# Kernel optimization log

Hardware: AMD Instinct MI355X
Metric: run time of the kernel (lower is better)

## Reference

```python
import jax, jax.numpy as jnp
import numpy as np

IN_FEATURES = 2048
N_CONCEPTS = 64
EMB_SIZE = 128
BATCH = 8192
NEG_SLOPE = 0.01  # torch LeakyReLU default


def _leaky_relu(x):
    return jnp.where(x >= 0, x, NEG_SLOPE * x)


def setup_inputs() -> dict:
    key = jax.random.key(0)
    ks = jax.random.split(key, 7)
    s_e = 1.0 / np.sqrt(IN_FEATURES)
    s_c = 1.0 / np.sqrt(EMB_SIZE)
    s_p = 1.0 / np.sqrt(2 * EMB_SIZE)
    return {
        "x": jax.random.normal(ks[0], (BATCH, IN_FEATURES), jnp.float32),
        # embedder: Linear(in_features, emb_size)
        "We": jax.random.uniform(ks[1], (EMB_SIZE, IN_FEATURES), jnp.float32, -s_e, s_e),
        "be": jax.random.uniform(ks[2], (EMB_SIZE,), jnp.float32, -s_e, s_e),
        # per-concept generators: K x Linear(emb_size, 2*emb_size)
        "Wc": jax.random.uniform(ks[3], (N_CONCEPTS, 2 * EMB_SIZE, EMB_SIZE), jnp.float32, -s_c, s_c),
        "bc": jax.random.uniform(ks[4], (N_CONCEPTS, 2 * EMB_SIZE), jnp.float32, -s_c, s_c),
        # shared prob predictor: Linear(2*emb_size, 1)
        "wp": jax.random.uniform(ks[5], (2 * EMB_SIZE,), jnp.float32, -s_p, s_p),
        "bp": jax.random.uniform(ks[6], (1,), jnp.float32, -s_p, s_p),
    }


def reference(x, We, be, Wc, bc, wp, bp):
    # emb_pre: [B, E]
    emb = _leaky_relu(x @ We.T + be)
    # per-concept contexts, batched GEMM: [B, K, 2E]
    context = _leaky_relu(jnp.einsum("be,khe->bkh", emb, Wc) + bc)
    # concept probabilities: [B, K]
    c_pred = jax.nn.sigmoid(jnp.einsum("bkh,h->bk", context, wp) + bp[0])
    # no interventions (c=None) -> c_int == c_pred
    c_int = c_pred
    context_pos = context[:, :, :EMB_SIZE]
    context_neg = context[:, :, EMB_SIZE:]
    g = c_pred[:, :, None]
    c_emb = context_pos * g + context_neg * (1.0 - g)  # [B, K, E]
    return c_emb, c_pred, c_int, emb
```

## Files before the change

kernel.cpp:

```cpp
#include <hip/hip_runtime.h>
#include <hip/hip_bf16.h>

#define IN_F   2048
#define N_CON  64
#define EMB    128
#define BATCH  8192

#define CEMB_OFF  0
#define CPRED_OFF 67108864
#define CINT_OFF  67633152
#define EMB_OFF   68157440

typedef __attribute__((ext_vector_type(4))) float f32x4;
typedef __attribute__((ext_vector_type(8))) short short8;
typedef __attribute__((ext_vector_type(4))) short short4v;

#define MFMA16(A,B,C) __builtin_amdgcn_mfma_f32_16x16x32_bf16((A),(B),(C),0,0,0)

__device__ __forceinline__ short f2bf(float f) {
  unsigned u = __float_as_uint(f);
  u += 0x7FFFu + ((u >> 16) & 1u);
  return (short)(u >> 16);
}

__device__ __forceinline__ void gload_lds16(const void* g, void* l) {
  __builtin_amdgcn_global_load_lds(
      (const __attribute__((address_space(1))) unsigned*)g,
      (__attribute__((address_space(3))) unsigned*)l, 16, 0, 0);
}

__global__ void conv2_kernel(const float* __restrict__ a, short* __restrict__ da, int n4a,
                             const float* __restrict__ b, short* __restrict__ db, int n4b) {
  int i = blockIdx.x * blockDim.x + threadIdx.x;
  const float* s; short* d; int j;
  if (i < n4a)            { s = a; d = da; j = i; }
  else if (i < n4a + n4b) { s = b; d = db; j = i - n4a; }
  else return;
  f32x4 v = *(const f32x4*)(s + (size_t)j * 4);
  short4v o;
  o.x = f2bf(v.x); o.y = f2bf(v.y); o.z = f2bf(v.z); o.w = f2bf(v.w);
  *(short4v*)(d + (size_t)j * 4) = o;
}

__global__ __launch_bounds__(256, 4)
void gemm1_kernel(const float* __restrict__ x,
                  const short* __restrict__ we_bf,
                  const float* __restrict__ be,
                  float* __restrict__ out_emb,
                  short* __restrict__ emb_bf) {
  __shared__ short As[32 * 128];
  __shared__ short Bs[128 * 128];

  const int t = threadIdx.x;
  const int w = t >> 6, l = t & 63;
  const int row0 = blockIdx.x * 32;

  f32x4 acc[2][2];
#pragma unroll
  for (int i = 0; i < 2; ++i)
#pragma unroll
    for (int j = 0; j < 2; ++j) acc[i][j] = (f32x4){0.f, 0.f, 0.f, 0.f};

  const int ar = t >> 3;
  const int as = t & 7;
  const float* xrow = x + (size_t)(row0 + ar) * IN_F + as * 16;

  const int brl = t >> 4;
  const int bseg = l & 15;

  for (int kt = 0; kt < 16; ++kt) {
    const int k0 = kt * 128;
#pragma unroll
    for (int h = 0; h < 2; ++h) {
      f32x4 v0 = *(const f32x4*)(xrow + k0 + h * 8);
      f32x4 v1 = *(const f32x4*)(xrow + k0 + h * 8 + 4);
      short8 o;
      o[0] = f2bf(v0.x); o[1] = f2bf(v0.y); o[2] = f2bf(v0.z); o[3] = f2bf(v0.w);
      o[4] = f2bf(v1.x); o[5] = f2bf(v1.y); o[6] = f2bf(v1.z); o[7] = f2bf(v1.w);
      int col = (as * 16 + h * 8) ^ ((ar & 7) << 3);
      *(short8*)&As[ar * 128 + col] = o;
    }
#pragma unroll
    for (int i = 0; i < 8; ++i) {
      int n = i * 16 + brl;
      const short* src = we_bf + (size_t)n * IN_F + k0 + ((bseg ^ (n & 7)) * 8);
      gload_lds16(src, &Bs[i * 2048 + w * 512]);
    }
    __syncthreads();
#pragma unroll
    for (int ks = 0; ks < 4; ++ks) {
      int kcol = ks * 32 + ((l >> 4) << 3);
      int r0 = l & 15, r1 = 16 + (l & 15);
      short8 a0 = *(const short8*)&As[r0 * 128 + (kcol ^ ((r0 & 7) << 3))];
      short8 a1 = *(const short8*)&As[r1 * 128 + (kcol ^ ((r1 & 7) << 3))];
      int n0 = w * 32 + (l & 15), n1 = w * 32 + 16 + (l & 15);
      short8 b0 = *(const short8*)&Bs[n0 * 128 + (kcol ^ ((n0 & 7) << 3))];
      short8 b1 = *(const short8*)&Bs[n1 * 128 + (kcol ^ ((n1 & 7) << 3))];
      acc[0][0] = MFMA16(a0, b0, acc[0][0]);
      acc[1][0] = MFMA16(a1, b0, acc[1][0]);
      acc[0][1] = MFMA16(a0, b1, acc[0][1]);
      acc[1][1] = MFMA16(a1, b1, acc[1][1]);
    }
    __syncthreads();
  }

#pragma unroll
  for (int nf = 0; nf < 2; ++nf) {
    int e = w * 32 + nf * 16 + (l & 15);
    float bev = be[e];
#pragma unroll
    for (int mf = 0; mf < 2; ++mf) {
#pragma unroll
      for (int r = 0; r < 4; ++r) {
        int b = row0 + mf * 16 + ((l >> 4) << 2) + r;
        float v = acc[mf][nf][r] + bev;
        v = v >= 0.f ? v : 0.01f * v;
        out_emb[(size_t)b * EMB + e] = v;
        emb_bf[(size_t)b * EMB + e] = f2bf(v);
      }
    }
  }
}

__global__ __launch_bounds__(512, 2)
void gemm2_kernel(const short* __restrict__ emb_bf,
                  const short* __restrict__ wc_bf,
                  const float* __restrict__ bc,
                  const float* __restrict__ wp,
                  const float* __restrict__ bp,
                  float* __restrict__ ws_pred,
                  float* __restrict__ out) {
  __shared__ short As[256 * 128];
  __shared__ short Bs[256 * 128];

  const int t = threadIdx.x;
  const int w = t >> 6, l = t & 63;
  const int kc = blockIdx.x & 63;
  const int mbase = (blockIdx.x >> 6) * 256;

  float wph[16], bcv[16];
#pragma unroll
  for (int nf = 0; nf < 16; ++nf) {
    wph[nf] = wp[nf * 16 + (l & 15)];
    bcv[nf] = bc[kc * 256 + nf * 16 + (l & 15)];
  }
  const float bp0 = bp[0];

  const int rl = t >> 4;
  const int seg = l & 15;
#pragma unroll
  for (int i = 0; i < 8; ++i) {
    int rA = i * 32 + rl;
    gload_lds16(emb_bf + (size_t)(mbase + rA) * 128 + ((seg ^ (rA & 7)) * 8),
                &As[i * 4096 + w * 512]);
  }
#pragma unroll
  for (int i = 0; i < 8; ++i) {
    int rB = i * 32 + rl;
    gload_lds16(wc_bf + (size_t)kc * 32768 + (size_t)rB * 128 + ((seg ^ (rB & 7)) * 8),
                &Bs[i * 4096 + w * 512]);
  }
  __syncthreads();

  f32x4 acc[2][16];
#pragma unroll
  for (int i = 0; i < 2; ++i)
#pragma unroll
    for (int j = 0; j < 16; ++j) acc[i][j] = (f32x4){0.f, 0.f, 0.f, 0.f};

  const int wr = w * 32;
#pragma unroll
  for (int ks = 0; ks < 4; ++ks) {
    int kcol = ks * 32 + ((l >> 4) << 3);
    int r0 = wr + (l & 15), r1 = wr + 16 + (l & 15);
    short8 a0 = *(const short8*)&As[r0 * 128 + (kcol ^ ((r0 & 7) << 3))];
    short8 a1 = *(const short8*)&As[r1 * 128 + (kcol ^ ((r1 & 7) << 3))];
#pragma unroll
    for (int nf = 0; nf < 16; ++nf) {
      int n = nf * 16 + (l & 15);
      short8 b = *(const short8*)&Bs[n * 128 + (kcol ^ ((n & 7) << 3))];
      acc[0][nf] = MFMA16(a0, b, acc[0][nf]);
      acc[1][nf] = MFMA16(a1, b, acc[1][nf]);
    }
  }

  float g[2][4];
#pragma unroll
  for (int mf = 0; mf < 2; ++mf) {
    f32x4 p = (f32x4){0.f, 0.f, 0.f, 0.f};
#pragma unroll
    for (int nf = 0; nf < 16; ++nf) {
#pragma unroll
      for (int r = 0; r < 4; ++r) {
        float v = acc[mf][nf][r] + bcv[nf];
        v = v >= 0.f ? v : 0.01f * v;
        acc[mf][nf][r] = v;
        p[r] += v * wph[nf];
      }
    }
#pragma unroll
    for (int r = 0; r < 4; ++r) {
      float s = p[r];
      s += __shfl_xor(s, 1);
      s += __shfl_xor(s, 2);
      s += __shfl_xor(s, 4);
      s += __shfl_xor(s, 8);
      g[mf][r] = 1.f / (1.f + __expf(-(s + bp0)));
    }
  }

  if ((l & 15) == 0) {
#pragma unroll
    for (int mf = 0; mf < 2; ++mf) {
      f32x4 gv;
      gv.x = g[mf][0]; gv.y = g[mf][1]; gv.z = g[mf][2]; gv.w = g[mf][3];
      *(f32x4*)&ws_pred[(size_t)kc * 8192 + mbase + wr + mf * 16 + ((l >> 4) << 2)] = gv;
    }
  }

#pragma unroll
  for (int mf = 0; mf < 2; ++mf) {
#pragma unroll
    for (int r = 0; r < 4; ++r) {
      int brow = mbase + wr + mf * 16 + ((l >> 4) << 2) + r;
      float gg = g[mf][r];
#pragma unroll
      for (int nf = 0; nf < 8; ++nf) {
        float v = acc[mf][nf][r] * gg + acc[mf][nf + 8][r] * (1.f - gg);
        out[(size_t)brow * 8192 + kc * 128 + nf * 16 + (l & 15)] = v;
      }
    }
  }
}

__global__ __launch_bounds__(256)
void pred_tr_kernel(const float* __restrict__ ws_pred, float* __restrict__ out) {
  __shared__ float T[64][65];
  const int t = threadIdx.x;
  const int b0 = blockIdx.x * 64;

  {
    int kc = t >> 2;
    int j0 = (t & 3) * 16;
    const float* src = ws_pred + (size_t)kc * 8192 + b0 + j0;
#pragma unroll
    for (int i = 0; i < 4; ++i) {
      f32x4 v = *(const f32x4*)(src + i * 4);
      T[kc][j0 + i * 4 + 0] = v.x;
      T[kc][j0 + i * 4 + 1] = v.y;
      T[kc][j0 + i * 4 + 2] = v.z;
      T[kc][j0 + i * 4 + 3] = v.w;
    }
  }
  __syncthreads();
  {
    int bl = t & 63;
    int kq = (t >> 6) * 16;
#pragma unroll
    for (int i = 0; i < 4; ++i) {
      f32x4 v;
      v.x = T[kq + i * 4 + 0][bl];
      v.y = T[kq + i * 4 + 1][bl];
      v.z = T[kq + i * 4 + 2][bl];
      v.w = T[kq + i * 4 + 3][bl];
      *(f32x4*)&out[CPRED_OFF + (size_t)(b0 + bl) * 64 + kq + i * 4] = v;
      *(f32x4*)&out[CINT_OFF + (size_t)(b0 + bl) * 64 + kq + i * 4] = v;
    }
  }
}

extern "C" void kernel_launch(void* const* d_in, const int* in_sizes, int n_in,
                              void* d_out, int out_size, void* d_ws, size_t ws_size,
                              hipStream_t stream) {
  (void)in_sizes; (void)n_in; (void)out_size; (void)ws_size;
  const float* x  = (const float*)d_in[0];
  const float* We = (const float*)d_in[1];
  const float* be = (const float*)d_in[2];
  const float* Wc = (const float*)d_in[3];
  const float* bc = (const float*)d_in[4];
  const float* wp = (const float*)d_in[5];
  const float* bp = (const float*)d_in[6];
  float* out = (float*)d_out;

  short* we_bf  = (short*)d_ws;
  short* wc_bf  = we_bf + 262144;
  short* emb_bf = wc_bf + 2097152;
  float* ws_pred = (float*)(emb_bf + 1048576);

  conv2_kernel<<<2304, 256, 0, stream>>>(We, we_bf, 65536, Wc, wc_bf, 524288);
  gemm1_kernel<<<256, 256, 0, stream>>>(x, we_bf, be, out + EMB_OFF, emb_bf);
  gemm2_kernel<<<2048, 512, 0, stream>>>(emb_bf, wc_bf, bc, wp, bp, ws_pred, out);
  pred_tr_kernel<<<128, 256, 0, stream>>>(ws_pred, out);
}
```

Baseline: 136.5 us.

## Keep concept weight tile resident and loop over batch chunks in gemm2

gemm2 now loads each concept's 256x128 weight tile into LDS once per block and iterates over eight 64-row batch chunks, reloading only the small activation tile each iteration. Grid drops from 2048 to 1024 blocks of 256 threads with fewer accumulators per thread. gemm1 is also retiled to 16-row blocks, doubling its grid to 512 blocks for better occupancy. The point is to cut redundant weight traffic and register pressure. The cost is a serialized chunk loop with extra barriers and little overlap between the activation reload and compute.

```diff
diff --git a/kernel.cpp b/kernel.cpp
--- a/kernel.cpp
+++ b/kernel.cpp
@@ -48,58 +48,52 @@
                   const float* __restrict__ be,
                   float* __restrict__ out_emb,
                   short* __restrict__ emb_bf) {
-  __shared__ short As[32 * 128];
+  __shared__ short As[16 * 128];
   __shared__ short Bs[128 * 128];
 
   const int t = threadIdx.x;
   const int w = t >> 6, l = t & 63;
-  const int row0 = blockIdx.x * 32;
-
-  f32x4 acc[2][2];
-#pragma unroll
-  for (int i = 0; i < 2; ++i)
-#pragma unroll
-    for (int j = 0; j < 2; ++j) acc[i][j] = (f32x4){0.f, 0.f, 0.f, 0.f};
-
-  const int ar = t >> 3;
-  const int as = t & 7;
-  const float* xrow = x + (size_t)(row0 + ar) * IN_F + as * 16;
+  const int row0 = blockIdx.x * 16;
+
+  f32x4 acc[2];
+  acc[0] = (f32x4){0.f, 0.f, 0.f, 0.f};
+  acc[1] = (f32x4){0.f, 0.f, 0.f, 0.f};
+
+  const int ar = t >> 4;
+  const int aseg = t & 15;
+  const float* xrow = x + (size_t)(row0 + ar) * IN_F + aseg * 8;
+  short* adst = &As[ar * 128 + ((aseg * 8) ^ ((ar & 7) << 3))];
 
   const int brl = t >> 4;
   const int bseg = l & 15;
 
   for (int kt = 0; kt < 16; ++kt) {
     const int k0 = kt * 128;
-#pragma unroll
-    for (int h = 0; h < 2; ++h) {
-      f32x4 v0 = *(const f32x4*)(xrow + k0 + h * 8);
-      f32x4 v1 = *(const f32x4*)(xrow + k0 + h * 8 + 4);
+    {
+      f32x4 v0 = *(const f32x4*)(xrow + k0);
+      f32x4 v1 = *(const f32x4*)(xrow + k0 + 4);
       short8 o;
       o[0] = f2bf(v0.x); o[1] = f2bf(v0.y); o[2] = f2bf(v0.z); o[3] = f2bf(v0.w);
       o[4] = f2bf(v1.x); o[5] = f2bf(v1.y); o[6] = f2bf(v1.z); o[7] = f2bf(v1.w);
-      int col = (as * 16 + h * 8) ^ ((ar & 7) << 3);
-      *(short8*)&As[ar * 128 + col] = o;
+      *(short8*)adst = o;
     }
 #pragma unroll
     for (int i = 0; i < 8; ++i) {
       int n = i * 16 + brl;
-      const short* src = we_bf + (size_t)n * IN_F + k0 + ((bseg ^ (n & 7)) * 8);
-      gload_lds16(src, &Bs[i * 2048 + w * 512]);
+      gload_lds16(we_bf + (size_t)n * IN_F + k0 + ((bseg ^ (n & 7)) * 8),
+                  &Bs[i * 2048 + w * 512]);
     }
     __syncthreads();
 #pragma unroll
     for (int ks = 0; ks < 4; ++ks) {
       int kcol = ks * 32 + ((l >> 4) << 3);
-      int r0 = l & 15, r1 = 16 + (l & 15);
-      short8 a0 = *(const short8*)&As[r0 * 128 + (kcol ^ ((r0 & 7) << 3))];
-      short8 a1 = *(const short8*)&As[r1 * 128 + (kcol ^ ((r1 & 7) << 3))];
-      int n0 = w * 32 + (l & 15), n1 = w * 32 + 16 + (l & 15);
+      int r0 = l & 15;
+      short8 a = *(const short8*)&As[r0 * 128 + (kcol ^ ((r0 & 7) << 3))];
+      int n0 = w * 32 + (l & 15), n1 = n0 + 16;
       short8 b0 = *(const short8*)&Bs[n0 * 128 + (kcol ^ ((n0 & 7) << 3))];
       short8 b1 = *(const short8*)&Bs[n1 * 128 + (kcol ^ ((n1 & 7) << 3))];
-      acc[0][0] = MFMA16(a0, b0, acc[0][0]);
-      acc[1][0] = MFMA16(a1, b0, acc[1][0]);
-      acc[0][1] = MFMA16(a0, b1, acc[0][1]);
-      acc[1][1] = MFMA16(a1, b1, acc[1][1]);
+      acc[0] = MFMA16(a, b0, acc[0]);
+      acc[1] = MFMA16(a, b1, acc[1]);
     }
     __syncthreads();
   }
@@ -109,20 +103,17 @@
     int e = w * 32 + nf * 16 + (l & 15);
     float bev = be[e];
 #pragma unroll
-    for (int mf = 0; mf < 2; ++mf) {
-#pragma unroll
-      for (int r = 0; r < 4; ++r) {
-        int b = row0 + mf * 16 + ((l >> 4) << 2) + r;
-        float v = acc[mf][nf][r] + bev;
-        v = v >= 0.f ? v : 0.01f * v;
-        out_emb[(size_t)b * EMB + e] = v;
-        emb_bf[(size_t)b * EMB + e] = f2bf(v);
-      }
-    }
-  }
-}
-
-__global__ __launch_bounds__(512, 2)
+    for (int r = 0; r < 4; ++r) {
+      int b = row0 + ((l >> 4) << 2) + r;
+      float v = acc[nf][r] + bev;
+      v = v >= 0.f ? v : 0.01f * v;
+      out_emb[(size_t)b * EMB + e] = v;
+      emb_bf[(size_t)b * EMB + e] = f2bf(v);
+    }
+  }
+}
+
+__global__ __launch_bounds__(256, 2)
 void gemm2_kernel(const short* __restrict__ emb_bf,
                   const short* __restrict__ wc_bf,
                   const float* __restrict__ bc,
@@ -130,13 +121,13 @@
                   const float* __restrict__ bp,
                   float* __restrict__ ws_pred,
                   float* __restrict__ out) {
-  __shared__ short As[256 * 128];
   __shared__ short Bs[256 * 128];
+  __shared__ short As[64 * 128];
 
   const int t = threadIdx.x;
   const int w = t >> 6, l = t & 63;
   const int kc = blockIdx.x & 63;
-  const int mbase = (blockIdx.x >> 6) * 256;
+  const int mch = (blockIdx.x >> 6) * 512;
 
   float wph[16], bcv[16];
 #pragma unroll
@@ -148,56 +139,62 @@
 
   const int rl = t >> 4;
   const int seg = l & 15;
-#pragma unroll
-  for (int i = 0; i < 8; ++i) {
-    int rA = i * 32 + rl;
-    gload_lds16(emb_bf + (size_t)(mbase + rA) * 128 + ((seg ^ (rA & 7)) * 8),
-                &As[i * 4096 + w * 512]);
-  }
-#pragma unroll
-  for (int i = 0; i < 8; ++i) {
-    int rB = i * 32 + rl;
+
+#pragma unroll
+  for (int i = 0; i < 16; ++i) {
+    int rB = i * 16 + rl;
     gload_lds16(wc_bf + (size_t)kc * 32768 + (size_t)rB * 128 + ((seg ^ (rB & 7)) * 8),
-                &Bs[i * 4096 + w * 512]);
-  }
-  __syncthreads();
-
-  f32x4 acc[2][16];
-#pragma unroll
-  for (int i = 0; i < 2; ++i)
-#pragma unroll
-    for (int j = 0; j < 16; ++j) acc[i][j] = (f32x4){0.f, 0.f, 0.f, 0.f};
-
-  const int wr = w * 32;
-#pragma unroll
-  for (int ks = 0; ks < 4; ++ks) {
-    int kcol = ks * 32 + ((l >> 4) << 3);
-    int r0 = wr + (l & 15), r1 = wr + 16 + (l & 15);
-    short8 a0 = *(const short8*)&As[r0 * 128 + (kcol ^ ((r0 & 7) << 3))];
-    short8 a1 = *(const short8*)&As[r1 * 128 + (kcol ^ ((r1 & 7) << 3))];
+                &Bs[i * 2048 + w * 512]);
+  }
+#pragma unroll
+  for (int i = 0; i < 4; ++i) {
+    int rA = i * 16 + rl;
+    gload_lds16(emb_bf + (size_t)(mch + rA) * 128 + ((seg ^ (rA & 7)) * 8),
+                &As[i * 2048 + w * 512]);
+  }
+
+  for (int it = 0; it < 8; ++it) {
+    __syncthreads();
+
+    f32x4 acc[16];
+#pragma unroll
+    for (int j = 0; j < 16; ++j) acc[j] = (f32x4){0.f, 0.f, 0.f, 0.f};
+
+    const int r0 = w * 16 + (l & 15);
+#pragma unroll
+    for (int ks = 0; ks < 4; ++ks) {
+      int kcol = ks * 32 + ((l >> 4) << 3);
+      short8 a = *(const short8*)&As[r0 * 128 + (kcol ^ ((r0 & 7) << 3))];
+#pragma unroll
+      for (int nf = 0; nf < 16; ++nf) {
+        int n = nf * 16 + (l & 15);
+        short8 b = *(const short8*)&Bs[n * 128 + (kcol ^ ((n & 7) << 3))];
+        acc[nf] = MFMA16(a, b, acc[nf]);
+      }
+    }
+    __syncthreads();
+
+    if (it < 7) {
+#pragma unroll
+      for (int i = 0; i < 4; ++i) {
+        int rA = i * 16 + rl;
+        gload_lds16(emb_bf + (size_t)(mch + (it + 1) * 64 + rA) * 128 + ((seg ^ (rA & 7)) * 8),
+                    &As[i * 2048 + w * 512]);
+      }
+    }
+
+    f32x4 p = (f32x4){0.f, 0.f, 0.f, 0.f};
 #pragma unroll
     for (int nf = 0; nf < 16; ++nf) {
-      int n = nf * 16 + (l & 15);
-      short8 b = *(const short8*)&Bs[n * 128 + (kcol ^ ((n & 7) << 3))];
-      acc[0][nf] = MFMA16(a0, b, acc[0][nf]);
-      acc[1][nf] = MFMA16(a1, b, acc[1][nf]);
-    }
-  }
-
-  float g[2][4];
-#pragma unroll
-  for (int mf = 0; mf < 2; ++mf) {
-    f32x4 p = (f32x4){0.f, 0.f, 0.f, 0.f};
-#pragma unroll
-    for (int nf = 0; nf < 16; ++nf) {
 #pragma unroll
       for (int r = 0; r < 4; ++r) {
-        float v = acc[mf][nf][r] + bcv[nf];
+        float v = acc[nf][r] + bcv[nf];
         v = v >= 0.f ? v : 0.01f * v;
-        acc[mf][nf][r] = v;
+        acc[nf][r] = v;
         p[r] += v * wph[nf];
       }
     }
+    float g[4];
 #pragma unroll
     for (int r = 0; r < 4; ++r) {
       float s = p[r];
@@ -205,28 +202,21 @@
       s += __shfl_xor(s, 2);
       s += __shfl_xor(s, 4);
       s += __shfl_xor(s, 8);
-      g[mf][r] = 1.f / (1.f + __expf(-(s + bp0)));
-    }
-  }
-
-  if ((l & 15) == 0) {
-#pragma unroll
-    for (int mf = 0; mf < 2; ++mf) {
-      f32x4 gv;
-      gv.x = g[mf][0]; gv.y = g[mf][1]; gv.z = g[mf][2]; gv.w = g[mf][3];
-      *(f32x4*)&ws_pred[(size_t)kc * 8192 + mbase + wr + mf * 16 + ((l >> 4) << 2)] = gv;
-    }
-  }
-
-#pragma unroll
-  for (int mf = 0; mf < 2; ++mf) {
+      g[r] = 1.f / (1.f + __expf(-(s + bp0)));
+    }
+
+    const int rowb = mch + it * 64 + w * 16 + ((l >> 4) << 2);
+    if ((l & 15) == 0) {
+      f32x4 gv; gv.x = g[0]; gv.y = g[1]; gv.z = g[2]; gv.w = g[3];
+      *(f32x4*)&ws_pred[(size_t)kc * 8192 + rowb] = gv;
+    }
 #pragma unroll
     for (int r = 0; r < 4; ++r) {
-      int brow = mbase + wr + mf * 16 + ((l >> 4) << 2) + r;
-      float gg = g[mf][r];
+      int brow = rowb + r;
+      float gg = g[r];
 #pragma unroll
       for (int nf = 0; nf < 8; ++nf) {
-        float v = acc[mf][nf][r] * gg + acc[mf][nf + 8][r] * (1.f - gg);
+        float v = acc[nf][r] * gg + acc[nf + 8][r] * (1.f - gg);
         out[(size_t)brow * 8192 + kc * 128 + nf * 16 + (l & 15)] = v;
       }
     }
@@ -288,7 +278,7 @@
   float* ws_pred = (float*)(emb_bf + 1048576);
 
   conv2_kernel<<<2304, 256, 0, stream>>>(We, we_bf, 65536, Wc, wc_bf, 524288);
-  gemm1_kernel<<<256, 256, 0, stream>>>(x, we_bf, be, out + EMB_OFF, emb_bf);
-  gemm2_kernel<<<2048, 512, 0, stream>>>(emb_bf, wc_bf, bc, wp, bp, ws_pred, out);
+  gemm1_kernel<<<512, 256, 0, stream>>>(x, we_bf, be, out + EMB_OFF, emb_bf);
+  gemm2_kernel<<<1024, 256, 0, stream>>>(emb_bf, wc_bf, bc, wp, bp, ws_pred, out);
   pred_tr_kernel<<<128, 256, 0, stream>>>(ws_pred, out);
 }
```

Result: faster. 124.5 us (-8.7%).
